# Optimization experiments

Measured on AMD Instinct MI355X. Metric: run time of the kernel, lower is better.

Reference implementation:

```python
import jax, jax.numpy as jnp
import numpy as np

N, F_DIM, H_DIM = 8192, 128, 128

def setup_inputs() -> dict:
    key = jax.random.key(0)
    ks = jax.random.split(key, 7)
    inp = {
        "input": jax.random.normal(ks[0], (N, F_DIM), dtype=jnp.float32),
        "wavelets": jax.random.normal(ks[1], (N, N), dtype=jnp.float32) / np.sqrt(N),
        "wavelets_inv": jax.random.normal(ks[2], (N, N), dtype=jnp.float32) / np.sqrt(N),
        # layer 1 params
        "W1": jax.random.uniform(ks[3], (F_DIM, H_DIM), dtype=jnp.float32,
                                 minval=-np.sqrt(6.0/(F_DIM+H_DIM)), maxval=np.sqrt(6.0/(F_DIM+H_DIM))),
        "f1": jax.random.uniform(ks[4], (N,), dtype=jnp.float32, minval=0.9, maxval=1.1),
        # layer 2 params
        "W2": jax.random.uniform(ks[5], (H_DIM, H_DIM), dtype=jnp.float32,
                                 minval=-np.sqrt(6.0/(H_DIM+H_DIM)), maxval=np.sqrt(6.0/(H_DIM+H_DIM))),
        "f2": jax.random.uniform(ks[6], (N,), dtype=jnp.float32, minval=0.9, maxval=1.1),
    }
    return inp

def _gwnn_layer(features, wavelets, wavelets_inv, W, filt):
    # torch: wavelets @ diag(filt) @ (wavelets_inv @ (features @ W))
    # diag(filt) matmul == column-wise scale of wavelets (broadcast elementwise)
    xw = features @ W                      # [N, out]
    spec = wavelets_inv @ xw               # [N, out] spectral-domain features
    spec = filt[:, None] * spec            # apply learnable diagonal filter
    return wavelets @ spec                 # [N, out]

def reference(input, wavelets, wavelets_inv, W1, f1, W2, f2):
    # eval mode: dropout is identity
    h1 = jax.nn.relu(_gwnn_layer(input, wavelets, wavelets_inv, W1, f1))
    out = _gwnn_layer(h1, wavelets, wavelets_inv, W2, f2)
    return out
```

## Files before the change

### kernel.cpp

```cpp
#include <hip/hip_runtime.h>
#include <hip/hip_bf16.h>
#include <stdint.h>


typedef __attribute__((ext_vector_type(4))) float f32x4;
typedef __attribute__((ext_vector_type(8))) short s16x8;
typedef __attribute__((ext_vector_type(4))) short s16x4;

#define DEVI static __device__ __forceinline__

DEVI short bf1(float x){ __bf16 h = (__bf16)x; return __builtin_bit_cast(short, h); }

DEVI s16x8 cvt8(f32x4 lo, f32x4 hi){
  s16x8 r;
#pragma unroll
  for (int i = 0; i < 4; ++i){ r[i] = bf1(lo[i]); r[4+i] = bf1(hi[i]); }
  return r;
}

DEVI void glds16(const void* g, void* l){
  __builtin_amdgcn_global_load_lds((const __attribute__((address_space(1))) void*)g,
                                   (__attribute__((address_space(3))) void*)l, 16, 0, 0);
}

template<int N> DEVI void waitvm(){
  if constexpr (N == 0)       asm volatile("s_waitcnt vmcnt(0)"  ::: "memory");
  else if constexpr (N == 5)  asm volatile("s_waitcnt vmcnt(5)"  ::: "memory");
  else if constexpr (N == 6)  asm volatile("s_waitcnt vmcnt(6)"  ::: "memory");
  else if constexpr (N == 10) asm volatile("s_waitcnt vmcnt(10)" ::: "memory");
  else if constexpr (N == 12) asm volatile("s_waitcnt vmcnt(12)" ::: "memory");
  else if constexpr (N == 15) asm volatile("s_waitcnt vmcnt(15)" ::: "memory");
  else if constexpr (N == 18) asm volatile("s_waitcnt vmcnt(18)" ::: "memory");
  else if constexpr (N == 20) asm volatile("s_waitcnt vmcnt(20)" ::: "memory");
  else if constexpr (N == 24) asm volatile("s_waitcnt vmcnt(24)" ::: "memory");
}

template<bool ABF, bool SCALE, bool RELU, int OUTM>
__global__ __launch_bounds__(256, 1) void gemm_k(
    const void* __restrict__ Ap, const short* __restrict__ Btp,
    const float* __restrict__ fp, void* __restrict__ Outp, int K, int M)
{
  constexpr int BM = 32, BN = 128, BK = 64;
  constexpr int ASZ = ABF ? BM*BK*2 : BM*BK*4;
  constexpr int BSZ = BN*BK*2;
  constexpr int TSZ = ASZ + BSZ;
  constexpr int NL  = ABF ? 5 : 6;
  constexpr int NBUF = 6;
  constexpr int PRE  = 5;
  __shared__ uint8_t lds[NBUF*TSZ];

  const int tid  = threadIdx.x;
  const int lane = tid & 63;
  const int wv   = tid >> 6;
  const int la   = lane & 15;
  const int g4   = lane >> 4;
  const int m0   = blockIdx.x * BM;

  const float* gA0 = nullptr; const float* gA1 = nullptr; const short* gAh = nullptr;
  if constexpr (!ABF){
    const float* Af = (const float*)Ap;
    int r0 = (wv<<3) + (lane>>4);
    int r1 = r0 + 4;
    gA0 = Af + (size_t)(m0+r0)*K + (((lane&15)^(r0&15))<<2);
    gA1 = Af + (size_t)(m0+r1)*K + (((lane&15)^(r1&15))<<2);
  } else {
    const short* Ah = (const short*)Ap;
    int r = (wv<<3) + (lane>>3);
    gAh = Ah + (size_t)(m0+r)*K + (((lane&7)^(r&7))<<3);
  }
  const int nb0 = (wv<<5) + (lane>>3);
  const short* gB0 = Btp + (size_t)(nb0    )*K + (((lane&7)^(nb0&7))<<3);
  const short* gB1 = Btp + (size_t)(nb0+ 8 )*K + (((lane&7)^(nb0&7))<<3);
  const short* gB2 = Btp + (size_t)(nb0+16 )*K + (((lane&7)^(nb0&7))<<3);
  const short* gB3 = Btp + (size_t)(nb0+24 )*K + (((lane&7)^(nb0&7))<<3);

  int aoff[2][2][2];
  int boff[2][2];
#pragma unroll
  for (int mi = 0; mi < 2; ++mi){
    const int r = mi*16 + la;
#pragma unroll
    for (int kf = 0; kf < 2; ++kf){
      if constexpr (!ABF){
        const int v0 = kf*8 + (g4<<1);
        aoff[mi][kf][0] = r*256 + (((v0  )^(r&15))<<4);
        aoff[mi][kf][1] = r*256 + (((v0+1)^(r&15))<<4);
      } else {
        const int u = kf*4 + g4;
        aoff[mi][kf][0] = r*128 + ((u^(r&7))<<4);
        aoff[mi][kf][1] = 0;
      }
    }
  }
#pragma unroll
  for (int ni = 0; ni < 2; ++ni){
    const int n = (wv<<5) + ni*16 + la;
#pragma unroll
    for (int kf = 0; kf < 2; ++kf){
      const int u = kf*4 + g4;
      boff[ni][kf] = n*128 + ((u^(n&7))<<4);
    }
  }

  f32x4 acc[2][2] = {};

  auto STAGE = [&](uint8_t* buf){
    uint8_t* Ab = buf;
    uint8_t* Bb = buf + ASZ;
    if constexpr (!ABF){
      glds16(gA0, Ab + (wv<<11));
      glds16(gA1, Ab + (wv<<11) + 1024);
      gA0 += BK; gA1 += BK;
    } else {
      glds16(gAh, Ab + (wv<<10));
      gAh += BK;
    }
    glds16(gB0, Bb + (wv<<12));
    glds16(gB1, Bb + (wv<<12) + 1024);
    glds16(gB2, Bb + (wv<<12) + 2048);
    glds16(gB3, Bb + (wv<<12) + 3072);
    gB0 += BK; gB1 += BK; gB2 += BK; gB3 += BK;
  };

  auto COMPUTE = [&](const uint8_t* buf){
    const uint8_t* Ab = buf;
    const uint8_t* Bb = buf + ASZ;
#pragma unroll
    for (int kf = 0; kf < 2; ++kf){
      s16x8 a0, a1, b0, b1;
      if constexpr (!ABF){
        a0 = cvt8(*(const f32x4*)(Ab + aoff[0][kf][0]), *(const f32x4*)(Ab + aoff[0][kf][1]));
        a1 = cvt8(*(const f32x4*)(Ab + aoff[1][kf][0]), *(const f32x4*)(Ab + aoff[1][kf][1]));
      } else {
        a0 = *(const s16x8*)(Ab + aoff[0][kf][0]);
        a1 = *(const s16x8*)(Ab + aoff[1][kf][0]);
      }
      b0 = *(const s16x8*)(Bb + boff[0][kf]);
      b1 = *(const s16x8*)(Bb + boff[1][kf]);
      acc[0][0] = __builtin_amdgcn_mfma_f32_16x16x32_bf16(a0, b0, acc[0][0], 0, 0, 0);
      acc[0][1] = __builtin_amdgcn_mfma_f32_16x16x32_bf16(a0, b1, acc[0][1], 0, 0, 0);
      acc[1][0] = __builtin_amdgcn_mfma_f32_16x16x32_bf16(a1, b0, acc[1][0], 0, 0, 0);
      acc[1][1] = __builtin_amdgcn_mfma_f32_16x16x32_bf16(a1, b1, acc[1][1], 0, 0, 0);
    }
  };

  const int nsteps = K >> 6;

  uint8_t* const lend = lds + NBUF*TSZ;
  uint8_t* bs = lds;
  uint8_t* bc = lds;

  for (int s = 0; s < PRE && s < nsteps; ++s){
    STAGE(bs);
    bs += TSZ; if (bs == lend) bs = lds;
  }

  for (int t = 0; t < nsteps; ++t){
    const int ahead = nsteps - 1 - t;
    if (ahead >= 4)      waitvm<4*NL>();
    else if (ahead == 3) waitvm<3*NL>();
    else if (ahead == 2) waitvm<2*NL>();
    else if (ahead == 1) waitvm<1*NL>();
    else                 waitvm<0>();
    __builtin_amdgcn_s_barrier();
    asm volatile("" ::: "memory");
    if (t + PRE < nsteps){
      STAGE(bs);
      bs += TSZ; if (bs == lend) bs = lds;
    }
    COMPUTE(bc);
    bc += TSZ; if (bc == lend) bc = lds;
    asm volatile("" ::: "memory");
  }

  const int mbase = m0 + (g4<<2);
  const int nc0   = (wv<<5) + la;
  f32x4 fv0, fv1;
  if constexpr (SCALE){
    fv0 = *(const f32x4*)(fp + mbase);
    fv1 = *(const f32x4*)(fp + mbase + 16);
  }
#pragma unroll
  for (int mi = 0; mi < 2; ++mi){
#pragma unroll
    for (int ni = 0; ni < 2; ++ni){
      f32x4 v = acc[mi][ni];
      if constexpr (SCALE) v = v * (mi ? fv1 : fv0);
      if constexpr (RELU){
#pragma unroll
        for (int r = 0; r < 4; ++r) v[r] = fmaxf(v[r], 0.0f);
      }
      if constexpr (OUTM == 2){
        s16x4 pk;
#pragma unroll
        for (int r = 0; r < 4; ++r) pk[r] = bf1(v[r]);
        *(s16x4*)((short*)Outp + (size_t)(nc0 + (ni<<4))*M + (mbase + (mi<<4))) = pk;
      } else if constexpr (OUTM == 1){
#pragma unroll
        for (int r = 0; r < 4; ++r)
          ((short*)Outp)[(size_t)(mbase + (mi<<4) + r)*BN + nc0 + (ni<<4)] = bf1(v[r]);
      } else {
#pragma unroll
        for (int r = 0; r < 4; ++r)
          ((float*)Outp)[(size_t)(mbase + (mi<<4) + r)*BN + nc0 + (ni<<4)] = v[r];
      }
    }
  }
}

__global__ void wtrans_k(const float* __restrict__ W1, const float* __restrict__ W2,
                         short* __restrict__ T1, short* __restrict__ T2){
  const int idx = blockIdx.x*256 + threadIdx.x;
  const int m = idx >> 14, rem = idx & 16383;
  const int n = rem >> 7, k = rem & 127;
  const float* W = m ? W2 : W1;
  short* T = m ? T2 : T1;
  T[n*128 + k] = bf1(W[k*128 + n]);
}

extern "C" void kernel_launch(void* const* d_in, const int* in_sizes, int n_in,
                              void* d_out, int out_size, void* d_ws, size_t ws_size,
                              hipStream_t stream){
  const float* input = (const float*)d_in[0];
  const float* wav   = (const float*)d_in[1];
  const float* winv  = (const float*)d_in[2];
  const float* W1    = (const float*)d_in[3];
  const float* f1    = (const float*)d_in[4];
  const float* W2    = (const float*)d_in[5];
  const float* f2    = (const float*)d_in[6];

  uint8_t* ws = (uint8_t*)d_ws;
  short* W1T = (short*)(ws);
  short* W2T = (short*)(ws + (32<<10));
  short* XWT = (short*)(ws + (64<<10));
  short* SPT = (short*)(ws + (64<<10) + (2<<20));
  short* H1  = (short*)(ws + (64<<10) + (4<<20));

  constexpr int M = 8192;
  dim3 b(256), g(M/32), gt(128);

  wtrans_k<<<gt, b, 0, stream>>>(W1, W2, W1T, W2T);
  gemm_k<false,false,false,2><<<g,b,0,stream>>>(input, W1T, nullptr, XWT, 128, M);
  gemm_k<false,true ,false,2><<<g,b,0,stream>>>(winv,  XWT, f1,      SPT, M,   M);
  gemm_k<false,false,true ,1><<<g,b,0,stream>>>(wav,   SPT, nullptr, H1,  M,   M);
  gemm_k<true ,false,false,2><<<g,b,0,stream>>>(H1,    W2T, nullptr, XWT, 128, M);
  gemm_k<false,true ,false,2><<<g,b,0,stream>>>(winv,  XWT, f2,      SPT, M,   M);
  gemm_k<false,false,false,0><<<g,b,0,stream>>>(wav,   SPT, nullptr, d_out, M, M);
}
```

Baseline: 326.8 us.

## Write bf16 copies of wavelet matrices in layer 1, reuse in layer 2

During the first layer's two big GEMMs, wave 0 of each block writes the bf16-converted A tiles of wavelets_inv and wavelets to workspace. The second layer then reads these bf16 copies instead of the fp32 originals, which halves its A-matrix read traffic. The pipeline depth also drops from 6 to 3 LDS buffers with a simpler wait scheme. The extra 256MB of writes in layer 1 and the reduced prefetch depth could offset the savings, and the path needs a large workspace.

Measured after the change: 361.2 us. +10.5%, slower.

```diff
diff --git a/kernel.cpp b/kernel.cpp
--- a/kernel.cpp
+++ b/kernel.cpp
@@ -28,25 +28,21 @@
   else if constexpr (N == 5)  asm volatile("s_waitcnt vmcnt(5)"  ::: "memory");
   else if constexpr (N == 6)  asm volatile("s_waitcnt vmcnt(6)"  ::: "memory");
   else if constexpr (N == 10) asm volatile("s_waitcnt vmcnt(10)" ::: "memory");
-  else if constexpr (N == 12) asm volatile("s_waitcnt vmcnt(12)" ::: "memory");
-  else if constexpr (N == 15) asm volatile("s_waitcnt vmcnt(15)" ::: "memory");
-  else if constexpr (N == 18) asm volatile("s_waitcnt vmcnt(18)" ::: "memory");
-  else if constexpr (N == 20) asm volatile("s_waitcnt vmcnt(20)" ::: "memory");
-  else if constexpr (N == 24) asm volatile("s_waitcnt vmcnt(24)" ::: "memory");
-}
-
-template<bool ABF, bool SCALE, bool RELU, int OUTM>
-__global__ __launch_bounds__(256, 1) void gemm_k(
+  else if constexpr (N == 14) asm volatile("s_waitcnt vmcnt(14)" ::: "memory");
+}
+
+template<bool ABF, bool WCOPY, bool SCALE, bool RELU, int OUTM>
+__global__ __launch_bounds__(256, 1) void ggemm(
     const void* __restrict__ Ap, const short* __restrict__ Btp,
-    const float* __restrict__ fp, void* __restrict__ Outp, int K, int M)
+    const float* __restrict__ fp, void* __restrict__ Outp,
+    short* __restrict__ Acp, int K, int M)
 {
   constexpr int BM = 32, BN = 128, BK = 64;
   constexpr int ASZ = ABF ? BM*BK*2 : BM*BK*4;
   constexpr int BSZ = BN*BK*2;
   constexpr int TSZ = ASZ + BSZ;
   constexpr int NL  = ABF ? 5 : 6;
-  constexpr int NBUF = 6;
-  constexpr int PRE  = 5;
+  constexpr int NBUF = 3, PRE = 2;
   __shared__ uint8_t lds[NBUF*TSZ];
 
   const int tid  = threadIdx.x;
@@ -55,6 +51,7 @@
   const int la   = lane & 15;
   const int g4   = lane >> 4;
   const int m0   = blockIdx.x * BM;
+  const bool w0u = (__builtin_amdgcn_readfirstlane(wv) == 0);
 
   const float* gA0 = nullptr; const float* gA1 = nullptr; const short* gAh = nullptr;
   if constexpr (!ABF){
@@ -74,6 +71,12 @@
   const short* gB2 = Btp + (size_t)(nb0+16 )*K + (((lane&7)^(nb0&7))<<3);
   const short* gB3 = Btp + (size_t)(nb0+24 )*K + (((lane&7)^(nb0&7))<<3);
 
+  short* wc0 = nullptr; short* wc1 = nullptr;
+  if constexpr (WCOPY){
+    wc0 = Acp + (size_t)(m0 + la)*K + (g4<<3);
+    wc1 = wc0 + (size_t)16*K;
+  }
+
   int aoff[2][2][2];
   int boff[2][2];
 #pragma unroll
@@ -131,6 +134,12 @@
       if constexpr (!ABF){
         a0 = cvt8(*(const f32x4*)(Ab + aoff[0][kf][0]), *(const f32x4*)(Ab + aoff[0][kf][1]));
         a1 = cvt8(*(const f32x4*)(Ab + aoff[1][kf][0]), *(const f32x4*)(Ab + aoff[1][kf][1]));
+        if constexpr (WCOPY){
+          if (w0u){
+            *(s16x8*)(wc0 + kf*32) = a0;
+            *(s16x8*)(wc1 + kf*32) = a1;
+          }
+        }
       } else {
         a0 = *(const s16x8*)(Ab + aoff[0][kf][0]);
         a1 = *(const s16x8*)(Ab + aoff[1][kf][0]);
@@ -142,29 +151,33 @@
       acc[1][0] = __builtin_amdgcn_mfma_f32_16x16x32_bf16(a1, b0, acc[1][0], 0, 0, 0);
       acc[1][1] = __builtin_amdgcn_mfma_f32_16x16x32_bf16(a1, b1, acc[1][1], 0, 0, 0);
     }
+    if constexpr (WCOPY){ wc0 += BK; wc1 += BK; }
   };
 
-  const int nsteps = K >> 6;
-
+  const int ns = K >> 6;
   uint8_t* const lend = lds + NBUF*TSZ;
   uint8_t* bs = lds;
   uint8_t* bc = lds;
-
-  for (int s = 0; s < PRE && s < nsteps; ++s){
+  for (int s = 0; s < PRE && s < ns; ++s){
     STAGE(bs);
     bs += TSZ; if (bs == lend) bs = lds;
   }
-
-  for (int t = 0; t < nsteps; ++t){
-    const int ahead = nsteps - 1 - t;
-    if (ahead >= 4)      waitvm<4*NL>();
-    else if (ahead == 3) waitvm<3*NL>();
-    else if (ahead == 2) waitvm<2*NL>();
-    else if (ahead == 1) waitvm<1*NL>();
-    else                 waitvm<0>();
+  for (int t = 0; t < ns; ++t){
+    if constexpr (WCOPY){
+      if (w0u){
+        if (t == 0)           waitvm<6>();
+        else if (t == 1)      waitvm<10>();
+        else if (t <= ns - 2) waitvm<14>();
+        else                  waitvm<0>();
+      } else {
+        if (t < ns - 1) waitvm<6>(); else waitvm<0>();
+      }
+    } else {
+      if (t < ns - 1) waitvm<NL>(); else waitvm<0>();
+    }
     __builtin_amdgcn_s_barrier();
     asm volatile("" ::: "memory");
-    if (t + PRE < nsteps){
+    if (t + PRE < ns){
       STAGE(bs);
       bs += TSZ; if (bs == lend) bs = lds;
     }
@@ -204,6 +217,149 @@
         for (int r = 0; r < 4; ++r)
           ((float*)Outp)[(size_t)(mbase + (mi<<4) + r)*BN + nc0 + (ni<<4)] = v[r];
       }
+    }
+  }
+}
+
+template<bool ABF>
+__global__ __launch_bounds__(256, 1) void sgemm(
+    const void* __restrict__ Ap, const short* __restrict__ Btp,
+    void* __restrict__ Outp, int K, int M)
+{
+  constexpr int BM = 32, BN = 128, BK = 64;
+  constexpr int ASZ = ABF ? BM*BK*2 : BM*BK*4;
+  constexpr int BSZ = BN*BK*2;
+  constexpr int TSZ = ASZ + BSZ;
+  constexpr int NL  = ABF ? 5 : 6;
+  constexpr int NBUF = 3, PRE = 2;
+  __shared__ uint8_t lds[NBUF*TSZ];
+
+  const int tid  = threadIdx.x;
+  const int lane = tid & 63;
+  const int wv   = tid >> 6;
+  const int la   = lane & 15;
+  const int g4   = lane >> 4;
+  const int m0   = blockIdx.x * BM;
+
+  const float* gA0 = nullptr; const float* gA1 = nullptr; const short* gAh = nullptr;
+  if constexpr (!ABF){
+    const float* Af = (const float*)Ap;
+    int r0 = (wv<<3) + (lane>>4);
+    int r1 = r0 + 4;
+    gA0 = Af + (size_t)(m0+r0)*K + (((lane&15)^(r0&15))<<2);
+    gA1 = Af + (size_t)(m0+r1)*K + (((lane&15)^(r1&15))<<2);
+  } else {
+    const short* Ah = (const short*)Ap;
+    int r = (wv<<3) + (lane>>3);
+    gAh = Ah + (size_t)(m0+r)*K + (((lane&7)^(r&7))<<3);
+  }
+  const int nb0 = (wv<<5) + (lane>>3);
+  const short* gB0 = Btp + (size_t)(nb0    )*K + (((lane&7)^(nb0&7))<<3);
+  const short* gB1 = Btp + (size_t)(nb0+ 8 )*K + (((lane&7)^(nb0&7))<<3);
+  const short* gB2 = Btp + (size_t)(nb0+16 )*K + (((lane&7)^(nb0&7))<<3);
+  const short* gB3 = Btp + (size_t)(nb0+24 )*K + (((lane&7)^(nb0&7))<<3);
+
+  int aoff[2][2][2];
+  int boff[2][2];
+#pragma unroll
+  for (int mi = 0; mi < 2; ++mi){
+    const int r = mi*16 + la;
+#pragma unroll
+    for (int kf = 0; kf < 2; ++kf){
+      if constexpr (!ABF){
+        const int v0 = kf*8 + (g4<<1);
+        aoff[mi][kf][0] = r*256 + (((v0  )^(r&15))<<4);
+        aoff[mi][kf][1] = r*256 + (((v0+1)^(r&15))<<4);
+      } else {
+        const int u = kf*4 + g4;
+        aoff[mi][kf][0] = r*128 + ((u^(r&7))<<4);
+        aoff[mi][kf][1] = 0;
+      }
+    }
+  }
+#pragma unroll
+  for (int ni = 0; ni < 2; ++ni){
+    const int n = (wv<<5) + ni*16 + la;
+#pragma unroll
+    for (int kf = 0; kf < 2; ++kf){
+      const int u = kf*4 + g4;
+      boff[ni][kf] = n*128 + ((u^(n&7))<<4);
+    }
+  }
+
+  f32x4 acc[2][2] = {};
+
+  auto STAGE = [&](uint8_t* buf){
+    uint8_t* Ab = buf;
+    uint8_t* Bb = buf + ASZ;
+    if constexpr (!ABF){
+      glds16(gA0, Ab + (wv<<11));
+      glds16(gA1, Ab + (wv<<11) + 1024);
+      gA0 += BK; gA1 += BK;
+    } else {
+      glds16(gAh, Ab + (wv<<10));
+      gAh += BK;
+    }
+    glds16(gB0, Bb + (wv<<12));
+    glds16(gB1, Bb + (wv<<12) + 1024);
+    glds16(gB2, Bb + (wv<<12) + 2048);
+    glds16(gB3, Bb + (wv<<12) + 3072);
+    gB0 += BK; gB1 += BK; gB2 += BK; gB3 += BK;
+  };
+
+  auto COMPUTE = [&](const uint8_t* buf){
+    const uint8_t* Ab = buf;
+    const uint8_t* Bb = buf + ASZ;
+#pragma unroll
+    for (int kf = 0; kf < 2; ++kf){
+      s16x8 a0, a1, b0, b1;
+      if constexpr (!ABF){
+        a0 = cvt8(*(const f32x4*)(Ab + aoff[0][kf][0]), *(const f32x4*)(Ab + aoff[0][kf][1]));
+        a1 = cvt8(*(const f32x4*)(Ab + aoff[1][kf][0]), *(const f32x4*)(Ab + aoff[1][kf][1]));
+      } else {
+        a0 = *(const s16x8*)(Ab + aoff[0][kf][0]);
+        a1 = *(const s16x8*)(Ab + aoff[1][kf][0]);
+      }
+      b0 = *(const s16x8*)(Bb + boff[0][kf]);
+      b1 = *(const s16x8*)(Bb + boff[1][kf]);
+      acc[0][0] = __builtin_amdgcn_mfma_f32_16x16x32_bf16(a0, b0, acc[0][0], 0, 0, 0);
+      acc[0][1] = __builtin_amdgcn_mfma_f32_16x16x32_bf16(a0, b1, acc[0][1], 0, 0, 0);
+      acc[1][0] = __builtin_amdgcn_mfma_f32_16x16x32_bf16(a1, b0, acc[1][0], 0, 0, 0);
+      acc[1][1] = __builtin_amdgcn_mfma_f32_16x16x32_bf16(a1, b1, acc[1][1], 0, 0, 0);
+    }
+  };
+
+  const int ns = K >> 6;
+  uint8_t* const lend = lds + NBUF*TSZ;
+  uint8_t* bs = lds;
+  uint8_t* bc = lds;
+  for (int s = 0; s < PRE && s < ns; ++s){
+    STAGE(bs);
+    bs += TSZ; if (bs == lend) bs = lds;
+  }
+  for (int t = 0; t < ns; ++t){
+    if (t < ns - 1) waitvm<NL>(); else waitvm<0>();
+    __builtin_amdgcn_s_barrier();
+    asm volatile("" ::: "memory");
+    if (t + PRE < ns){
+      STAGE(bs);
+      bs += TSZ; if (bs == lend) bs = lds;
+    }
+    COMPUTE(bc);
+    bc += TSZ; if (bc == lend) bc = lds;
+    asm volatile("" ::: "memory");
+  }
+
+  const int mbase = m0 + (g4<<2);
+  const int nc0   = (wv<<5) + la;
+#pragma unroll
+  for (int mi = 0; mi < 2; ++mi){
+#pragma unroll
+    for (int ni = 0; ni < 2; ++ni){
+      s16x4 pk;
+#pragma unroll
+      for (int r = 0; r < 4; ++r) pk[r] = bf1(acc[mi][ni][r]);
+      *(s16x4*)((short*)Outp + (size_t)(nc0 + (ni<<4))*M + (mbase + (mi<<4))) = pk;
     }
   }
 }
@@ -229,21 +385,33 @@
   const float* W2    = (const float*)d_in[5];
   const float* f2    = (const float*)d_in[6];
 
+  constexpr int M = 8192;
   uint8_t* ws = (uint8_t*)d_ws;
   short* W1T = (short*)(ws);
   short* W2T = (short*)(ws + (32<<10));
   short* XWT = (short*)(ws + (64<<10));
   short* SPT = (short*)(ws + (64<<10) + (2<<20));
   short* H1  = (short*)(ws + (64<<10) + (4<<20));
-
-  constexpr int M = 8192;
+  short* WI16 = (short*)(ws + (64<<10) + (6<<20));
+  short* WA16 = WI16 + (size_t)M*M;
+  const size_t needed = (64<<10) + (size_t)(6<<20) + 2*(size_t)M*M*2;
+  const bool big = (ws_size >= needed);
+
   dim3 b(256), g(M/32), gt(128);
 
   wtrans_k<<<gt, b, 0, stream>>>(W1, W2, W1T, W2T);
-  gemm_k<false,false,false,2><<<g,b,0,stream>>>(input, W1T, nullptr, XWT, 128, M);
-  gemm_k<false,true ,false,2><<<g,b,0,stream>>>(winv,  XWT, f1,      SPT, M,   M);
-  gemm_k<false,false,true ,1><<<g,b,0,stream>>>(wav,   SPT, nullptr, H1,  M,   M);
-  gemm_k<true ,false,false,2><<<g,b,0,stream>>>(H1,    W2T, nullptr, XWT, 128, M);
-  gemm_k<false,true ,false,2><<<g,b,0,stream>>>(winv,  XWT, f2,      SPT, M,   M);
-  gemm_k<false,false,false,0><<<g,b,0,stream>>>(wav,   SPT, nullptr, d_out, M, M);
-}
+  sgemm<false><<<g, b, 0, stream>>>(input, W1T, XWT, 128, M);
+  if (big){
+    ggemm<false,true ,true ,false,2><<<g,b,0,stream>>>(winv, XWT, f1, SPT, WI16, M, M);
+    ggemm<false,true ,false,true ,1><<<g,b,0,stream>>>(wav,  SPT, nullptr, H1, WA16, M, M);
+    sgemm<true ><<<g, b, 0, stream>>>(H1, W2T, XWT, 128, M);
+    ggemm<true ,false,true ,false,2><<<g,b,0,stream>>>(WI16, XWT, f2, SPT, nullptr, M, M);
+    ggemm<true ,false,false,false,0><<<g,b,0,stream>>>(WA16, SPT, nullptr, d_out, nullptr, M, M);
+  } else {
+    ggemm<false,false,true ,false,2><<<g,b,0,stream>>>(winv, XWT, f1, SPT, nullptr, M, M);
+    ggemm<false,false,false,true ,1><<<g,b,0,stream>>>(wav,  SPT, nullptr, H1, nullptr, M, M);
+    sgemm<true ><<<g, b, 0, stream>>>(H1, W2T, XWT, 128, M);
+    ggemm<false,false,true ,false,2><<<g,b,0,stream>>>(winv, XWT, f2, SPT, nullptr, M, M);
+    ggemm<false,false,false,false,0><<<g,b,0,stream>>>(wav,  SPT, nullptr, d_out, nullptr, M, M);
+  }
+}
```
